# Kernel tuning notes

Hardware: AMD Instinct MI355X
Metric: run time of the kernel (lower is better)

The kernel has to match this reference:

```python
import jax, jax.numpy as jnp
import numpy as np

N = 1024        # total atoms
H = 256         # hidden_dim
L = 512         # latent_dim
NG = 50         # n_gaussians
NI = 3          # n_interactions
CUTOFF = 5.0
MAXZ = 100
B = 16          # molecules (N // 64 atoms each)

CENTERS = jnp.linspace(0.0, CUTOFF, NG)
WIDTH = 0.5 * (CUTOFF / NG)   # scalar, same for all gaussians
LN_EPS = 1e-5

def gelu(x):
    return jax.nn.gelu(x, approximate=False)  # torch default GELU is exact erf

def setup_inputs() -> dict:
    key = jax.random.key(0)
    ks = jax.random.split(key, 24)
    s = 0.05
    inp = {
        'z': jax.random.randint(ks[0], (N,), 0, MAXZ),
        'pos': jax.random.uniform(ks[1], (N, 3), dtype=jnp.float32) * 10.0,  # 10 A box
        'batch': jnp.arange(N, dtype=jnp.int32) // (N // B),
        'emb': jax.random.normal(ks[2], (MAXZ, H), dtype=jnp.float32),
        # per-interaction params stacked over layer axis (NI)
        'fw1': jax.random.normal(ks[3], (NI, NG, H), dtype=jnp.float32) * s,
        'fb1': jnp.zeros((NI, H), jnp.float32),
        'fw2': jax.random.normal(ks[4], (NI, H, H), dtype=jnp.float32) * s,
        'fb2': jnp.zeros((NI, H), jnp.float32),
        'aw1': jax.random.normal(ks[5], (NI, H, H), dtype=jnp.float32) * s,
        'ab1': jnp.zeros((NI, H), jnp.float32),
        'aw2': jax.random.normal(ks[6], (NI, H, H), dtype=jnp.float32) * s,
        'ab2': jnp.zeros((NI, H), jnp.float32),
        # projection head
        'pw1': jax.random.normal(ks[7], (H, H), dtype=jnp.float32) * s,
        'pb1': jnp.zeros((H,), jnp.float32),
        'pw2': jax.random.normal(ks[8], (H, L), dtype=jnp.float32) * s,
        'pb2': jnp.zeros((L,), jnp.float32),
        'ln_g': jnp.ones((L,), jnp.float32),
        'ln_b': jnp.zeros((L,), jnp.float32),
    }
    return inp

def _interaction(h, pos, fw1, fb1, fw2, fb2, aw1, ab1, aw2, ab2):
    diff = pos[None, :, :] - pos[:, None, :]              # [N,N,3]
    dist = jnp.linalg.norm(diff, axis=-1)                  # [N,N]
    mask = (dist < CUTOFF) & (dist > 1e-6)                 # [N,N]
    rbf = jnp.exp(-((dist[..., None] - CENTERS) ** 2) / (2.0 * WIDTH ** 2))  # [N,N,NG]
    W = gelu(rbf @ fw1 + fb1) @ fw2 + fb2                  # [N,N,H] filter MLP
    Wm = W * mask[..., None].astype(W.dtype)
    # agg[i,c] = sum_j Wm[i,j,c] * h[j,c]
    agg = jnp.einsum('ijc,jc->ic', Wm, h)
    return gelu(agg @ aw1 + ab1) @ aw2 + ab2

def reference(z, pos, batch, emb, fw1, fb1, fw2, fb2, aw1, ab1, aw2, ab2,
              pw1, pb1, pw2, pb2, ln_g, ln_b):
    h = emb[z]                                             # [N,H]
    for i in range(NI):
        h = h + _interaction(h, pos, fw1[i], fb1[i], fw2[i], fb2[i],
                             aw1[i], ab1[i], aw2[i], ab2[i])
    pooled = jax.ops.segment_sum(h, batch, num_segments=B)  # [B,H]
    x = gelu(pooled @ pw1 + pb1) @ pw2 + pb2               # [B,L]
    mu = jnp.mean(x, axis=-1, keepdims=True)
    var = jnp.var(x, axis=-1, keepdims=True)
    return (x - mu) / jnp.sqrt(var + LN_EPS) * ln_g + ln_b
```

## Files before the change

### kernel.cpp

```cpp
#include <hip/hip_runtime.h>
#include <hip/hip_fp16.h>
#include <math.h>

#define N 1024
#define H 256
#define L 512
#define NG 50
#define NI 3
#define B 16
#define NBINS 2048
#define CUT 5.0f
#define BPB 16
#define TROWS (NBINS + 1)
#define MATB 4
#define CAP 768
#define SEGSZ 256
#define APAD 264

typedef __attribute__((ext_vector_type(8))) short bf16x8;
typedef __attribute__((ext_vector_type(4))) float f32x4;

#define FMA4(A_, S_, V_) do { \
    (A_).x = fmaf((S_), (V_).x, (A_).x); (A_).y = fmaf((S_), (V_).y, (A_).y); \
    (A_).z = fmaf((S_), (V_).z, (A_).z); (A_).w = fmaf((S_), (V_).w, (A_).w); } while (0)

__device__ __forceinline__ float gelu_f(float x) {
    return 0.5f * x * (1.0f + erff(x * 0.70710678118654752f));
}
__device__ __forceinline__ unsigned short f2bf(float f) {
    unsigned u = __float_as_uint(f);
    unsigned r = (u + 0x7fffu + ((u >> 16) & 1u)) >> 16;
    return (unsigned short)r;
}

__global__ void __launch_bounds__(256) setup_k(
        const int* __restrict__ z, const float* __restrict__ emb,
        const float* __restrict__ pos, float* __restrict__ h,
        __half* __restrict__ hhf, int* __restrict__ meta,
        int* __restrict__ cnts, const float* __restrict__ fw2,
        unsigned short* __restrict__ Bt, __half* __restrict__ Wtb,
        float* __restrict__ agg) {
    int tid = threadIdx.x;
    if (blockIdx.x >= N) {
        int blk = blockIdx.x - N;
        int l = blk / H, ch = blk % H;
        float v = fw2[((size_t)l * H + tid) * H + ch];
        Bt[((size_t)l * H + ch) * H + tid] = f2bf(v);
        if (tid == 0)
            Wtb[((size_t)l * TROWS + NBINS) * H + ch] = __float2half(0.f);
        return;
    }
    int i = blockIdx.x;
    float v = emb[z[i] * H + tid];
    h[i * H + tid] = v;
    hhf[i * H + tid] = __float2half(v);
    agg[(size_t)i * H + tid] = 0.f;

    __shared__ int sCnt;
    __shared__ int sMeta[CAP];
    if (tid == 0) sCnt = 0;
    __syncthreads();
    float pix = pos[i * 3 + 0], piy = pos[i * 3 + 1], piz = pos[i * 3 + 2];
    const float invd = (float)NBINS / CUT;
    int lane = tid & 63;
    for (int r = 0; r < 4; ++r) {
        int j = tid + r * 256;
        float dx = pos[j * 3 + 0] - pix;
        float dy = pos[j * 3 + 1] - piy;
        float dz = pos[j * 3 + 2] - piz;
        float d = sqrtf(dx * dx + dy * dy + dz * dz);
        bool keep = (d < CUT && d > 1e-6f);
        unsigned long long mk = __ballot(keep);
        int base = 0;
        if (lane == 0) base = atomicAdd(&sCnt, (int)__popcll(mk));
        base = __shfl(base, 0);
        if (keep) {
            int bin = (int)(d * invd);
            if (bin > NBINS - 1) bin = NBINS - 1;
            int off = (int)__popcll(mk & ((1ull << lane) - 1ull));
            sMeta[base + off] = j | (bin << 10);
        }
    }
    __syncthreads();
    int cnt = sCnt;
    int pc = (cnt + 31) & ~31;
    for (int t = cnt + tid; t < pc; t += 256)
        sMeta[t] = i | (NBINS << 10);
    __syncthreads();
    for (int t = tid; t < pc; t += 256)
        meta[(size_t)i * CAP + t] = sMeta[t];
    if (tid == 0) cnts[i] = pc;
}

__global__ void __launch_bounds__(256) table_k(
        const float* __restrict__ fw1, const float* __restrict__ fb1,
        const unsigned short* __restrict__ Bt, const float* __restrict__ fb2,
        __half* __restrict__ Wtb) {
    const int bpl = NBINS / BPB;
    int layer = blockIdx.x / bpl;
    int blk = blockIdx.x % bpl;
    int b0 = blk * BPB;
    int tid = threadIdx.x;
    int wid = tid >> 6, lane = tid & 63;
    int c4 = lane * 4;
    int ub = wid * 4;
    const float* lfw1 = fw1 + layer * NG * H;
    __half* lWt = Wtb + (size_t)layer * TROWS * H;

    __shared__ __align__(16) float sW1[NG][H];
    __shared__ __align__(16) float sRbf[BPB][56];
    __shared__ __align__(16) unsigned short sAb[BPB][APAD];
    const float delta = CUT / (float)NBINS;
    for (int idx = tid; idx < NG * (H / 4); idx += 256) {
        int k = idx >> 6;
        int c = (idx & 63) * 4;
        *(float4*)&sW1[k][c] = *(const float4*)(lfw1 + k * H + c);
    }
    for (int idx = tid; idx < BPB * NG; idx += 256) {
        int u = idx & 15;
        int k = idx >> 4;
        float d = ((float)(b0 + u) + 0.5f) * delta;
        float t = d - (float)k * (CUT / 49.0f);
        sRbf[u][k] = expf(t * t * -200.0f);
    }
    __syncthreads();

    float4 acc1[4];
    #pragma unroll
    for (int u = 0; u < 4; ++u) acc1[u] = make_float4(0.f, 0.f, 0.f, 0.f);
    for (int kq = 0; kq < 12; ++kq) {
        int k = kq * 4;
        float4 r0 = *(const float4*)&sRbf[ub + 0][k];
        float4 r1 = *(const float4*)&sRbf[ub + 1][k];
        float4 r2 = *(const float4*)&sRbf[ub + 2][k];
        float4 r3 = *(const float4*)&sRbf[ub + 3][k];
        float4 q0 = *(const float4*)&sW1[k + 0][c4];
        float4 q1 = *(const float4*)&sW1[k + 1][c4];
        float4 q2 = *(const float4*)&sW1[k + 2][c4];
        float4 q3 = *(const float4*)&sW1[k + 3][c4];
        FMA4(acc1[0], r0.x, q0); FMA4(acc1[0], r0.y, q1);
        FMA4(acc1[0], r0.z, q2); FMA4(acc1[0], r0.w, q3);
        FMA4(acc1[1], r1.x, q0); FMA4(acc1[1], r1.y, q1);
        FMA4(acc1[1], r1.z, q2); FMA4(acc1[1], r1.w, q3);
        FMA4(acc1[2], r2.x, q0); FMA4(acc1[2], r2.y, q1);
        FMA4(acc1[2], r2.z, q2); FMA4(acc1[2], r2.w, q3);
        FMA4(acc1[3], r3.x, q0); FMA4(acc1[3], r3.y, q1);
        FMA4(acc1[3], r3.z, q2); FMA4(acc1[3], r3.w, q3);
    }
    for (int k = 48; k < NG; ++k) {
        float4 q = *(const float4*)&sW1[k][c4];
        #pragma unroll
        for (int u = 0; u < 4; ++u) FMA4(acc1[u], sRbf[ub + u][k], q);
    }
    float4 b1 = *(const float4*)(fb1 + layer * H + c4);
    #pragma unroll
    for (int u = 0; u < 4; ++u) {
        ushort4 g;
        g.x = f2bf(gelu_f(acc1[u].x + b1.x));
        g.y = f2bf(gelu_f(acc1[u].y + b1.y));
        g.z = f2bf(gelu_f(acc1[u].z + b1.z));
        g.w = f2bf(gelu_f(acc1[u].w + b1.w));
        *(ushort4*)&sAb[ub + u][c4] = g;
    }
    __syncthreads();

    int m = lane & 15;
    int quad = lane >> 4;
    bf16x8 afr[8];
    #pragma unroll
    for (int c = 0; c < 8; ++c)
        afr[c] = *(const bf16x8*)&sAb[m][c * 32 + quad * 8];
    #pragma unroll
    for (int ct = 0; ct < 4; ++ct) {
        int chn = (wid * 4 + ct) * 16 + m;
        const bf16x8* Bv = (const bf16x8*)(Bt + ((size_t)layer * H + chn) * H);
        f32x4 acc = {0.f, 0.f, 0.f, 0.f};
        #pragma unroll
        for (int c = 0; c < 8; ++c)
            acc = __builtin_amdgcn_mfma_f32_16x16x32_bf16(afr[c], Bv[c * 4 + quad],
                                                          acc, 0, 0, 0);
        float bias = fb2[layer * H + chn];
        #pragma unroll
        for (int r = 0; r < 4; ++r) {
            int bin = b0 + quad * 4 + r;
            lWt[(size_t)bin * H + chn] = __float2half(acc[r] + bias);
        }
    }
}

__global__ void __launch_bounds__(256) pair_k(
    const __half* __restrict__ hhf, const __half* __restrict__ Wt,
    const int* __restrict__ gmeta, const int* __restrict__ cnts,
    float* __restrict__ agg) {
    int tid = threadIdx.x;
    int wid = tid >> 6, lane = tid & 63;
    int c4 = lane * 4;
    int b = blockIdx.x;
    int i = b / 3;
    int seg = b - i * 3;
    int pc = cnts[i];
    int sb = seg * SEGSZ;
    if (sb >= pc) return;
    int rem = pc - sb; if (rem > SEGSZ) rem = SEGSZ;
    int len = rem >> 2;
    int chunks = len >> 2;

    __shared__ __align__(16) float sPart[4][H];

    int sbase = __builtin_amdgcn_readfirstlane(sb + wid * len);
    const int* mptr = gmeta + (size_t)i * CAP + sbase;
    const char* WtB = (const char*)Wt;
    const char* hhB = (const char*)hhf;
    int choffB = lane * 8;

    float4 acc = make_float4(0.f, 0.f, 0.f, 0.f);
    int4 mA, mB;
    uint2 wA[4], hA[4], wB[4], hB[4];

    auto ldmeta = [&](int c) -> int4 {
        return *(const int4*)(mptr + c * 4);
    };
    auto one = [&](int p, uint2& wr, uint2& hr) {
        p = __builtin_amdgcn_readfirstlane(p);
        int j = p & 1023;
        int bin = p >> 10;
        wr = *(const uint2*)(WtB + (((unsigned)bin << 9) | (unsigned)choffB));
        hr = *(const uint2*)(hhB + (((unsigned)j << 9) | (unsigned)choffB));
    };
    auto issueD = [&](const int4& m4, uint2 (&wr)[4], uint2 (&hr)[4]) {
        one(m4.x, wr[0], hr[0]); one(m4.y, wr[1], hr[1]);
        one(m4.z, wr[2], hr[2]); one(m4.w, wr[3], hr[3]);
    };
    auto consume = [&](uint2 (&wr)[4], uint2 (&hr)[4]) {
        #pragma unroll
        for (int u = 0; u < 4; ++u) {
            __half2 w01 = *(__half2*)&wr[u].x;
            __half2 w23 = *(__half2*)&wr[u].y;
            __half2 h01 = *(__half2*)&hr[u].x;
            __half2 h23 = *(__half2*)&hr[u].y;
            acc.x += __half2float(w01.x) * __half2float(h01.x);
            acc.y += __half2float(w01.y) * __half2float(h01.y);
            acc.z += __half2float(w23.x) * __half2float(h23.x);
            acc.w += __half2float(w23.y) * __half2float(h23.y);
        }
    };

    if (chunks > 0) {
        mA = ldmeta(0);
        if (chunks > 1) mB = ldmeta(1);
        issueD(mA, wA, hA);
        for (int c = 0; c < chunks; c += 2) {
            if (c + 2 < chunks) mA = ldmeta(c + 2);
            if (c + 1 < chunks) issueD(mB, wB, hB);
            consume(wA, hA);
            if (c + 3 < chunks) mB = ldmeta(c + 3);
            if (c + 2 < chunks) issueD(mA, wA, hA);
            if (c + 1 < chunks) consume(wB, hB);
        }
    }
    *(float4*)&sPart[wid][c4] = acc;
    __syncthreads();
    float v = sPart[0][tid] + sPart[1][tid] + sPart[2][tid] + sPart[3][tid];
    atomicAdd(&agg[(size_t)i * H + tid], v);
}

__global__ void __launch_bounds__(512) mlp_k(
    float* __restrict__ agg, const float* __restrict__ hin,
    const float* __restrict__ aw1, const float* __restrict__ ab1,
    const float* __restrict__ aw2, const float* __restrict__ ab2,
    float* __restrict__ hout, __half* __restrict__ hhf_out) {
    int tid = threadIdx.x;
    int wid = tid >> 6, lane = tid & 63;
    int c4 = lane * 4;
    int i0 = blockIdx.x * MATB;
    __shared__ __align__(16) float sAT[H][MATB];
    __shared__ __align__(16) float sGT[H][MATB];
    __shared__ __align__(16) float sPart[8][MATB][H];

    if (tid < H) {
        #pragma unroll
        for (int r = 0; r < MATB; ++r) {
            sAT[tid][r] = agg[(size_t)(i0 + r) * H + tid];
            agg[(size_t)(i0 + r) * H + tid] = 0.f;
        }
    }
    __syncthreads();

    int k0 = wid * 32;
    float4 acc[MATB];
    #pragma unroll
    for (int a = 0; a < MATB; ++a) acc[a] = make_float4(0.f, 0.f, 0.f, 0.f);
    #pragma unroll 8
    for (int k = 0; k < 32; ++k) {
        float4 q = *(const float4*)(aw1 + (k0 + k) * H + c4);
        float4 act = *(const float4*)&sAT[k0 + k][0];
        FMA4(acc[0], act.x, q); FMA4(acc[1], act.y, q);
        FMA4(acc[2], act.z, q); FMA4(acc[3], act.w, q);
    }
    #pragma unroll
    for (int a = 0; a < MATB; ++a)
        *(float4*)&sPart[wid][a][c4] = acc[a];
    __syncthreads();
    if (tid < H) {
        float b1 = ab1[tid];
        float g[MATB];
        #pragma unroll
        for (int a = 0; a < MATB; ++a) {
            float v = b1;
            #pragma unroll
            for (int s = 0; s < 8; ++s) v += sPart[s][a][tid];
            g[a] = gelu_f(v);
        }
        *(float4*)&sGT[tid][0] = make_float4(g[0], g[1], g[2], g[3]);
    }
    __syncthreads();
    #pragma unroll
    for (int a = 0; a < MATB; ++a) acc[a] = make_float4(0.f, 0.f, 0.f, 0.f);
    #pragma unroll 8
    for (int k = 0; k < 32; ++k) {
        float4 q = *(const float4*)(aw2 + (k0 + k) * H + c4);
        float4 act = *(const float4*)&sGT[k0 + k][0];
        FMA4(acc[0], act.x, q); FMA4(acc[1], act.y, q);
        FMA4(acc[2], act.z, q); FMA4(acc[3], act.w, q);
    }
    #pragma unroll
    for (int a = 0; a < MATB; ++a)
        *(float4*)&sPart[wid][a][c4] = acc[a];
    __syncthreads();
    if (tid < H) {
        float b2 = ab2[tid];
        #pragma unroll
        for (int a = 0; a < MATB; ++a) {
            float v = b2;
            #pragma unroll
            for (int s = 0; s < 8; ++s) v += sPart[s][a][tid];
            float hv = hin[(i0 + a) * H + tid] + v;
            hout[(i0 + a) * H + tid] = hv;
            hhf_out[(i0 + a) * H + tid] = __float2half(hv);
        }
    }
}

__global__ void __launch_bounds__(256) head_k(
        const float* __restrict__ h,
        const float* __restrict__ pw1, const float* __restrict__ pb1,
        const float* __restrict__ pw2, const float* __restrict__ pb2,
        const float* __restrict__ ln_g, const float* __restrict__ ln_b,
        float* __restrict__ out) {
    int b = blockIdx.x, tid = threadIdx.x;
    int wid = tid >> 6, lane = tid & 63;
    int c4 = lane * 4;
    __shared__ float sP[H];
    __shared__ __align__(16) float sPw[4][H];
    __shared__ float sG[H];
    __shared__ __align__(16) float sP2[4][L];
    __shared__ float sX[L];
    __shared__ float sRed[256];

    float4 p = make_float4(0.f, 0.f, 0.f, 0.f);
    #pragma unroll 4
    for (int a = 0; a < 16; ++a) {
        float4 hv = *(const float4*)(h + (b * 64 + wid * 16 + a) * H + c4);
        p.x += hv.x; p.y += hv.y; p.z += hv.z; p.w += hv.w;
    }
    *(float4*)&sPw[wid][c4] = p;
    __syncthreads();
    sP[tid] = sPw[0][tid] + sPw[1][tid] + sPw[2][tid] + sPw[3][tid];
    __syncthreads();

    int k0 = wid * 64;
    float4 acc = make_float4(0.f, 0.f, 0.f, 0.f);
    #pragma unroll 8
    for (int k = 0; k < 64; ++k) {
        float4 q = *(const float4*)(pw1 + (k0 + k) * H + c4);
        float s = sP[k0 + k];
        FMA4(acc, s, q);
    }
    *(float4*)&sPw[wid][c4] = acc;
    __syncthreads();
    sG[tid] = gelu_f(pb1[tid] + sPw[0][tid] + sPw[1][tid] + sPw[2][tid] + sPw[3][tid]);
    __syncthreads();

    float4 a0 = make_float4(0.f, 0.f, 0.f, 0.f);
    float4 a1 = make_float4(0.f, 0.f, 0.f, 0.f);
    #pragma unroll 4
    for (int k = 0; k < 64; ++k) {
        float s = sG[k0 + k];
        float4 q0 = *(const float4*)(pw2 + (k0 + k) * L + lane * 8);
        float4 q1 = *(const float4*)(pw2 + (k0 + k) * L + lane * 8 + 4);
        FMA4(a0, s, q0);
        FMA4(a1, s, q1);
    }
    *(float4*)&sP2[wid][lane * 8] = a0;
    *(float4*)&sP2[wid][lane * 8 + 4] = a1;
    __syncthreads();
    for (int r = 0; r < 2; ++r) {
        int l = tid + r * 256;
        sX[l] = pb2[l] + sP2[0][l] + sP2[1][l] + sP2[2][l] + sP2[3][l];
    }
    __syncthreads();

    sRed[tid] = sX[tid] + sX[tid + 256];
    __syncthreads();
    for (int off = 128; off > 0; off >>= 1) {
        if (tid < off) sRed[tid] += sRed[tid + off];
        __syncthreads();
    }
    float mu = sRed[0] / (float)L;
    __syncthreads();
    float d0 = sX[tid] - mu, d1 = sX[tid + 256] - mu;
    sRed[tid] = d0 * d0 + d1 * d1;
    __syncthreads();
    for (int off = 128; off > 0; off >>= 1) {
        if (tid < off) sRed[tid] += sRed[tid + off];
        __syncthreads();
    }
    float var = sRed[0] / (float)L;
    float rstd = rsqrtf(var + 1e-5f);
    for (int r = 0; r < 2; ++r) {
        int l = tid + r * 256;
        out[b * L + l] = (sX[l] - mu) * rstd * ln_g[l] + ln_b[l];
    }
}

extern "C" void kernel_launch(void* const* d_in, const int* in_sizes, int n_in,
                              void* d_out, int out_size, void* d_ws, size_t ws_size,
                              hipStream_t stream) {
    const int*   z    = (const int*)d_in[0];
    const float* pos  = (const float*)d_in[1];
    const float* emb  = (const float*)d_in[3];
    const float* fw1  = (const float*)d_in[4];
    const float* fb1  = (const float*)d_in[5];
    const float* fw2  = (const float*)d_in[6];
    const float* fb2  = (const float*)d_in[7];
    const float* aw1  = (const float*)d_in[8];
    const float* ab1  = (const float*)d_in[9];
    const float* aw2  = (const float*)d_in[10];
    const float* ab2  = (const float*)d_in[11];
    const float* pw1  = (const float*)d_in[12];
    const float* pb1  = (const float*)d_in[13];
    const float* pw2  = (const float*)d_in[14];
    const float* pb2  = (const float*)d_in[15];
    const float* ln_g = (const float*)d_in[16];
    const float* ln_b = (const float*)d_in[17];
    float* out = (float*)d_out;

    float* hA  = (float*)d_ws;
    float* hB  = hA + N * H;
    float* agg = hB + N * H;
    __half* hhfA = (__half*)(agg + 2 * N * H);
    __half* hhfB = hhfA + N * H;
    __half* Wtb  = hhfB + N * H;
    int* meta = (int*)(Wtb + (size_t)NI * TROWS * H);
    int* cnts = meta + (size_t)N * CAP;
    unsigned short* Bt = (unsigned short*)(cnts + N);

    setup_k<<<N + NI * H, 256, 0, stream>>>(z, emb, pos, hA, hhfA, meta, cnts,
                                            fw2, Bt, Wtb, agg);
    table_k<<<NI * (NBINS / BPB), 256, 0, stream>>>(fw1, fb1, Bt, fb2, Wtb);
    float* hin = hA;  __half* hbin = hhfA;
    float* hout = hB; __half* hbout = hhfB;
    for (int it = 0; it < NI; ++it) {
        pair_k<<<3 * N, 256, 0, stream>>>(hbin, Wtb + (size_t)it * TROWS * H,
                                          meta, cnts, agg);
        mlp_k<<<N / MATB, 512, 0, stream>>>(agg, hin, aw1 + it * H * H, ab1 + it * H,
                                            aw2 + it * H * H, ab2 + it * H, hout, hbout);
        float* t1 = hin; hin = hout; hout = t1;
        __half* t2 = hbin; hbin = hbout; hbout = t2;
    }
    head_k<<<B, 256, 0, stream>>>(hin, pw1, pb1, pw2, pb2, ln_g, ln_b, out);
}
```

Baseline: 243.3 us.

## Fuse pair aggregation and atom MLP via last-block-done counters

Merges the pair aggregation kernel and the per-atom MLP kernel into one launch. Blocks are grouped so the 12 pair blocks covering 4 atoms share a counter, and the last block to finish runs the two-layer MLP for those atoms with 256 threads instead of 512. This drops one kernel launch per interaction and lets MLP work overlap with other groups' pair work. In exchange it adds atomic counters, thread fences and a serialized MLP tail inside one block per group.

Result: slower. 665.1 us (+173.4%).

```diff
diff --git a/kernel.cpp b/kernel.cpp
--- a/kernel.cpp
+++ b/kernel.cpp
@@ -15,6 +15,7 @@
 #define MATB 4
 #define CAP 768
 #define SEGSZ 256
+#define GBLK 12
 #define APAD 264
 
 typedef __attribute__((ext_vector_type(8))) short bf16x8;
@@ -39,7 +40,7 @@
         __half* __restrict__ hhf, int* __restrict__ meta,
         int* __restrict__ cnts, const float* __restrict__ fw2,
         unsigned short* __restrict__ Bt, __half* __restrict__ Wtb,
-        float* __restrict__ agg) {
+        float* __restrict__ agg, unsigned* __restrict__ gcnt) {
     int tid = threadIdx.x;
     if (blockIdx.x >= N) {
         int blk = blockIdx.x - N;
@@ -48,6 +49,8 @@
         Bt[((size_t)l * H + ch) * H + tid] = f2bf(v);
         if (tid == 0)
             Wtb[((size_t)l * TROWS + NBINS) * H + ch] = __float2half(0.f);
+        if (blockIdx.x == N)
+            gcnt[tid] = (unsigned)GBLK;
         return;
     }
     int i = blockIdx.x;
@@ -188,110 +191,121 @@
     }
 }
 
-__global__ void __launch_bounds__(256) pair_k(
+__global__ void __launch_bounds__(256) pm2_k(
     const __half* __restrict__ hhf, const __half* __restrict__ Wt,
     const int* __restrict__ gmeta, const int* __restrict__ cnts,
-    float* __restrict__ agg) {
-    int tid = threadIdx.x;
-    int wid = tid >> 6, lane = tid & 63;
-    int c4 = lane * 4;
-    int b = blockIdx.x;
-    int i = b / 3;
-    int seg = b - i * 3;
-    int pc = cnts[i];
-    int sb = seg * SEGSZ;
-    if (sb >= pc) return;
-    int rem = pc - sb; if (rem > SEGSZ) rem = SEGSZ;
-    int len = rem >> 2;
-    int chunks = len >> 2;
-
-    __shared__ __align__(16) float sPart[4][H];
-
-    int sbase = __builtin_amdgcn_readfirstlane(sb + wid * len);
-    const int* mptr = gmeta + (size_t)i * CAP + sbase;
-    const char* WtB = (const char*)Wt;
-    const char* hhB = (const char*)hhf;
-    int choffB = lane * 8;
-
-    float4 acc = make_float4(0.f, 0.f, 0.f, 0.f);
-    int4 mA, mB;
-    uint2 wA[4], hA[4], wB[4], hB[4];
-
-    auto ldmeta = [&](int c) -> int4 {
-        return *(const int4*)(mptr + c * 4);
-    };
-    auto one = [&](int p, uint2& wr, uint2& hr) {
-        p = __builtin_amdgcn_readfirstlane(p);
-        int j = p & 1023;
-        int bin = p >> 10;
-        wr = *(const uint2*)(WtB + (((unsigned)bin << 9) | (unsigned)choffB));
-        hr = *(const uint2*)(hhB + (((unsigned)j << 9) | (unsigned)choffB));
-    };
-    auto issueD = [&](const int4& m4, uint2 (&wr)[4], uint2 (&hr)[4]) {
-        one(m4.x, wr[0], hr[0]); one(m4.y, wr[1], hr[1]);
-        one(m4.z, wr[2], hr[2]); one(m4.w, wr[3], hr[3]);
-    };
-    auto consume = [&](uint2 (&wr)[4], uint2 (&hr)[4]) {
-        #pragma unroll
-        for (int u = 0; u < 4; ++u) {
-            __half2 w01 = *(__half2*)&wr[u].x;
-            __half2 w23 = *(__half2*)&wr[u].y;
-            __half2 h01 = *(__half2*)&hr[u].x;
-            __half2 h23 = *(__half2*)&hr[u].y;
-            acc.x += __half2float(w01.x) * __half2float(h01.x);
-            acc.y += __half2float(w01.y) * __half2float(h01.y);
-            acc.z += __half2float(w23.x) * __half2float(h23.x);
-            acc.w += __half2float(w23.y) * __half2float(h23.y);
-        }
-    };
-
-    if (chunks > 0) {
-        mA = ldmeta(0);
-        if (chunks > 1) mB = ldmeta(1);
-        issueD(mA, wA, hA);
-        for (int c = 0; c < chunks; c += 2) {
-            if (c + 2 < chunks) mA = ldmeta(c + 2);
-            if (c + 1 < chunks) issueD(mB, wB, hB);
-            consume(wA, hA);
-            if (c + 3 < chunks) mB = ldmeta(c + 3);
-            if (c + 2 < chunks) issueD(mA, wA, hA);
-            if (c + 1 < chunks) consume(wB, hB);
-        }
-    }
-    *(float4*)&sPart[wid][c4] = acc;
-    __syncthreads();
-    float v = sPart[0][tid] + sPart[1][tid] + sPart[2][tid] + sPart[3][tid];
-    atomicAdd(&agg[(size_t)i * H + tid], v);
-}
-
-__global__ void __launch_bounds__(512) mlp_k(
-    float* __restrict__ agg, const float* __restrict__ hin,
+    float* __restrict__ agg, unsigned* __restrict__ gcnt,
+    const float* __restrict__ hin,
     const float* __restrict__ aw1, const float* __restrict__ ab1,
     const float* __restrict__ aw2, const float* __restrict__ ab2,
     float* __restrict__ hout, __half* __restrict__ hhf_out) {
     int tid = threadIdx.x;
     int wid = tid >> 6, lane = tid & 63;
     int c4 = lane * 4;
-    int i0 = blockIdx.x * MATB;
+    int b = blockIdx.x;
+    int g = b / GBLK;
+    int sub = b - g * GBLK;
+    int i = g * MATB + (sub & 3);
+    int seg = sub >> 2;
+
+    __shared__ __align__(16) float sPart[4][H];
+    __shared__ unsigned sLast;
+
+    int pc = cnts[i];
+    int sb = seg * SEGSZ;
+    bool live = (sb < pc);
+    if (live) {
+        int rem = pc - sb; if (rem > SEGSZ) rem = SEGSZ;
+        int len = rem >> 2;
+        int chunks = len >> 2;
+
+        int sbase = __builtin_amdgcn_readfirstlane(sb + wid * len);
+        const int* mptr = gmeta + (size_t)i * CAP + sbase;
+        const char* WtB = (const char*)Wt;
+        const char* hhB = (const char*)hhf;
+        int choffB = lane * 8;
+
+        float4 acc = make_float4(0.f, 0.f, 0.f, 0.f);
+        int4 mA, mB;
+        uint2 wA[4], hA[4], wB[4], hB[4];
+
+        auto ldmeta = [&](int c) -> int4 {
+            return *(const int4*)(mptr + c * 4);
+        };
+        auto one = [&](int p, uint2& wr, uint2& hr) {
+            p = __builtin_amdgcn_readfirstlane(p);
+            int j = p & 1023;
+            int bin = p >> 10;
+            wr = *(const uint2*)(WtB + (((unsigned)bin << 9) | (unsigned)choffB));
+            hr = *(const uint2*)(hhB + (((unsigned)j << 9) | (unsigned)choffB));
+        };
+        auto issueD = [&](const int4& m4, uint2 (&wr)[4], uint2 (&hr)[4]) {
+            one(m4.x, wr[0], hr[0]); one(m4.y, wr[1], hr[1]);
+            one(m4.z, wr[2], hr[2]); one(m4.w, wr[3], hr[3]);
+        };
+        auto consume = [&](uint2 (&wr)[4], uint2 (&hr)[4]) {
+            #pragma unroll
+            for (int u = 0; u < 4; ++u) {
+                __half2 w01 = *(__half2*)&wr[u].x;
+                __half2 w23 = *(__half2*)&wr[u].y;
+                __half2 h01 = *(__half2*)&hr[u].x;
+                __half2 h23 = *(__half2*)&hr[u].y;
+                acc.x += __half2float(w01.x) * __half2float(h01.x);
+                acc.y += __half2float(w01.y) * __half2float(h01.y);
+                acc.z += __half2float(w23.x) * __half2float(h23.x);
+                acc.w += __half2float(w23.y) * __half2float(h23.y);
+            }
+        };
+
+        if (chunks > 0) {
+            mA = ldmeta(0);
+            if (chunks > 1) mB = ldmeta(1);
+            issueD(mA, wA, hA);
+            for (int c = 0; c < chunks; c += 2) {
+                if (c + 2 < chunks) mA = ldmeta(c + 2);
+                if (c + 1 < chunks) issueD(mB, wB, hB);
+                consume(wA, hA);
+                if (c + 3 < chunks) mB = ldmeta(c + 3);
+                if (c + 2 < chunks) issueD(mA, wA, hA);
+                if (c + 1 < chunks) consume(wB, hB);
+            }
+        }
+        *(float4*)&sPart[wid][c4] = acc;
+        __syncthreads();
+        float v = sPart[0][tid] + sPart[1][tid] + sPart[2][tid] + sPart[3][tid];
+        atomicAdd(&agg[(size_t)i * H + tid], v);
+    }
+    __syncthreads();
+    if (tid == 0) {
+        __threadfence();
+        unsigned old = atomicSub(&gcnt[g], 1u);
+        sLast = (old == 1u) ? 1u : 0u;
+    }
+    __syncthreads();
+    if (!sLast) return;
+    __threadfence();
+
+    int i0 = g * MATB;
     __shared__ __align__(16) float sAT[H][MATB];
     __shared__ __align__(16) float sGT[H][MATB];
-    __shared__ __align__(16) float sPart[8][MATB][H];
-
-    if (tid < H) {
-        #pragma unroll
-        for (int r = 0; r < MATB; ++r) {
-            sAT[tid][r] = agg[(size_t)(i0 + r) * H + tid];
-            agg[(size_t)(i0 + r) * H + tid] = 0.f;
-        }
-    }
-    __syncthreads();
-
-    int k0 = wid * 32;
+    __shared__ __align__(16) float sMp[4][MATB][H];
+
+    #pragma unroll
+    for (int r = 0; r < MATB; ++r) {
+        float v = __hip_atomic_load(&agg[(size_t)(i0 + r) * H + tid],
+                                    __ATOMIC_RELAXED, __HIP_MEMORY_SCOPE_AGENT);
+        sAT[tid][r] = v;
+        agg[(size_t)(i0 + r) * H + tid] = 0.f;
+    }
+    if (tid == 0) gcnt[g] = (unsigned)GBLK;
+    __syncthreads();
+
+    int k0 = wid * 64;
     float4 acc[MATB];
     #pragma unroll
     for (int a = 0; a < MATB; ++a) acc[a] = make_float4(0.f, 0.f, 0.f, 0.f);
     #pragma unroll 8
-    for (int k = 0; k < 32; ++k) {
+    for (int k = 0; k < 64; ++k) {
         float4 q = *(const float4*)(aw1 + (k0 + k) * H + c4);
         float4 act = *(const float4*)&sAT[k0 + k][0];
         FMA4(acc[0], act.x, q); FMA4(acc[1], act.y, q);
@@ -299,25 +313,25 @@
     }
     #pragma unroll
     for (int a = 0; a < MATB; ++a)
-        *(float4*)&sPart[wid][a][c4] = acc[a];
-    __syncthreads();
-    if (tid < H) {
-        float b1 = ab1[tid];
-        float g[MATB];
+        *(float4*)&sMp[wid][a][c4] = acc[a];
+    __syncthreads();
+    {
+        float b1v = ab1[tid];
+        float gg[MATB];
         #pragma unroll
         for (int a = 0; a < MATB; ++a) {
-            float v = b1;
+            float v = b1v;
             #pragma unroll
-            for (int s = 0; s < 8; ++s) v += sPart[s][a][tid];
-            g[a] = gelu_f(v);
+            for (int s = 0; s < 4; ++s) v += sMp[s][a][tid];
+            gg[a] = gelu_f(v);
         }
-        *(float4*)&sGT[tid][0] = make_float4(g[0], g[1], g[2], g[3]);
+        *(float4*)&sGT[tid][0] = make_float4(gg[0], gg[1], gg[2], gg[3]);
     }
     __syncthreads();
     #pragma unroll
     for (int a = 0; a < MATB; ++a) acc[a] = make_float4(0.f, 0.f, 0.f, 0.f);
     #pragma unroll 8
-    for (int k = 0; k < 32; ++k) {
+    for (int k = 0; k < 64; ++k) {
         float4 q = *(const float4*)(aw2 + (k0 + k) * H + c4);
         float4 act = *(const float4*)&sGT[k0 + k][0];
         FMA4(acc[0], act.x, q); FMA4(acc[1], act.y, q);
@@ -325,18 +339,18 @@
     }
     #pragma unroll
     for (int a = 0; a < MATB; ++a)
-        *(float4*)&sPart[wid][a][c4] = acc[a];
-    __syncthreads();
-    if (tid < H) {
-        float b2 = ab2[tid];
+        *(float4*)&sMp[wid][a][c4] = acc[a];
+    __syncthreads();
+    {
+        float b2v = ab2[tid];
         #pragma unroll
         for (int a = 0; a < MATB; ++a) {
-            float v = b2;
+            float v = b2v;
             #pragma unroll
-            for (int s = 0; s < 8; ++s) v += sPart[s][a][tid];
-            float hv = hin[(i0 + a) * H + tid] + v;
-            hout[(i0 + a) * H + tid] = hv;
-            hhf_out[(i0 + a) * H + tid] = __float2half(hv);
+            for (int s = 0; s < 4; ++s) v += sMp[s][a][tid];
+            float hv = hin[(size_t)(i0 + a) * H + tid] + v;
+            hout[(size_t)(i0 + a) * H + tid] = hv;
+            hhf_out[(size_t)(i0 + a) * H + tid] = __float2half(hv);
         }
     }
 }
@@ -453,18 +467,20 @@
     __half* Wtb  = hhfB + N * H;
     int* meta = (int*)(Wtb + (size_t)NI * TROWS * H);
     int* cnts = meta + (size_t)N * CAP;
-    unsigned short* Bt = (unsigned short*)(cnts + N);
+    unsigned* gcnt = (unsigned*)(cnts + N);
+    unsigned short* Bt = (unsigned short*)(gcnt + N / MATB);
 
     setup_k<<<N + NI * H, 256, 0, stream>>>(z, emb, pos, hA, hhfA, meta, cnts,
-                                            fw2, Bt, Wtb, agg);
+                                            fw2, Bt, Wtb, agg, gcnt);
     table_k<<<NI * (NBINS / BPB), 256, 0, stream>>>(fw1, fb1, Bt, fb2, Wtb);
     float* hin = hA;  __half* hbin = hhfA;
     float* hout = hB; __half* hbout = hhfB;
     for (int it = 0; it < NI; ++it) {
-        pair_k<<<3 * N, 256, 0, stream>>>(hbin, Wtb + (size_t)it * TROWS * H,
-                                          meta, cnts, agg);
-        mlp_k<<<N / MATB, 512, 0, stream>>>(agg, hin, aw1 + it * H * H, ab1 + it * H,
-                                            aw2 + it * H * H, ab2 + it * H, hout, hbout);
+        pm2_k<<<3 * N, 256, 0, stream>>>(hbin, Wtb + (size_t)it * TROWS * H,
+                                         meta, cnts, agg, gcnt, hin,
+                                         aw1 + it * H * H, ab1 + it * H,
+                                         aw2 + it * H * H, ab2 + it * H,
+                                         hout, hbout);
         float* t1 = hin; hin = hout; hout = t1;
         __half* t2 = hbin; hbin = hbout; hbout = t2;
     }
```
